# Optimization experiments

Measured on AMD Instinct MI355X. Metric: run time of the kernel, lower is better.

Reference implementation:

```python
import jax, jax.numpy as jnp
import numpy as np

N_ITEMS = 100000
EMB = 128
LAYERS = 3
N_EDGES = 1600000


def setup_inputs() -> dict:
    key = jax.random.key(0)
    k1, k2, k3, k4, k5 = jax.random.split(key, 5)
    embedding = jax.random.normal(k1, (N_ITEMS, EMB), dtype=jnp.float32)
    adj_vals = jax.random.uniform(k2, (N_EDGES,), dtype=jnp.float32)
    # per-layer Linear(emb, emb, bias=False) weights, torch default init scale ~ 1/sqrt(fan_in)
    weights = jax.random.normal(k3, (LAYERS, EMB, EMB), dtype=jnp.float32) / np.sqrt(EMB)
    rows = jax.random.randint(k4, (N_EDGES,), 0, N_ITEMS, dtype=jnp.int32)
    cols = jax.random.randint(k5, (N_EDGES,), 0, N_ITEMS, dtype=jnp.int32)
    return {"embedding": embedding, "adj_vals": adj_vals, "weights": weights,
            "rows": rows, "cols": cols}


def reference(embedding, adj_vals, weights, rows, cols):
    n = embedding.shape[0]
    layers = weights.shape[0]
    h = embedding
    acc = embedding  # final[0] = layer-0 embedding
    for i in range(layers):
        # Linear(bias=False): x @ W^T
        h = h @ weights[i].T
        # sparse.mm: out[r] = sum_e vals[e] * h[cols[e]] for edges with rows[e]==r
        msg = adj_vals[:, None] * h[cols]            # [E, D]
        h = jax.ops.segment_sum(msg, rows, num_segments=n)  # [N, D]
        # F.normalize(p=2, dim=-1): appended to final, but the UN-normalized h feeds the next layer
        norm = jnp.maximum(jnp.sqrt(jnp.sum(h * h, axis=-1, keepdims=True)), 1e-12)
        acc = acc + h / norm
    return acc / (layers + 1)
```

## Files before the change

kernel.cpp:

```cpp
#include <hip/hip_runtime.h>

#define N_ITEMS 100000
#define EMB     128
#define N_EDGES 1600000
#define NLAYERS 3
#define RCAP    48

typedef unsigned short u16;
typedef unsigned int   u32;
typedef __attribute__((ext_vector_type(8))) short short8;
typedef __attribute__((ext_vector_type(4))) float f32x4;

__device__ __forceinline__ float bf2f(u16 u) {
    union { u32 i; float f; } v; v.i = (u32)u << 16; return v.f;
}
__device__ __forceinline__ u16 f2bf(float f) {
    union { float f; u32 i; } v; v.f = f;
    u32 b = v.i;
    return (u16)((b + 0x7FFFu + ((b >> 16) & 1u)) >> 16);
}


__global__ __launch_bounds__(256) void fill_k(const int* __restrict__ rows,
                                              const int* __restrict__ cols,
                                              const float* __restrict__ vals,
                                              int* __restrict__ cnt,
                                              int2* __restrict__ bucket) {
    int e = blockIdx.x * 256 + threadIdx.x;
    if (e < N_EDGES) {
        int r = rows[e];
        int p = atomicAdd(&cnt[r], 1);
        if (p < RCAP) {
            bucket[(size_t)r * RCAP + p] = make_int2(cols[e], __float_as_int(vals[e]));
        }
    }
}


__global__ __launch_bounds__(256) void wconv_k(const float* __restrict__ W,
                                               u16* __restrict__ Wb) {
    int i = blockIdx.x * 256 + threadIdx.x;
    if (i < NLAYERS * EMB * EMB) Wb[i] = f2bf(W[i]);
}


__global__ __launch_bounds__(256) void init_k(const float4* __restrict__ emb,
                                              float4* __restrict__ out,
                                              ushort4* __restrict__ ebf) {
    int i = blockIdx.x * 256 + threadIdx.x;
    float4 v = emb[i];
    out[i] = make_float4(v.x * 0.25f, v.y * 0.25f, v.z * 0.25f, v.w * 0.25f);
    ushort4 u;
    u.x = f2bf(v.x); u.y = f2bf(v.y); u.z = f2bf(v.z); u.w = f2bf(v.w);
    ebf[i] = u;
}


__global__ __launch_bounds__(256) void gemm_k(const u16* __restrict__ in,
                                              const u16* __restrict__ Wb,
                                              u16* __restrict__ out) {
    __shared__ u16 Wl[128 * 136];
    int t = threadIdx.x;
    {
        int j = t >> 1, c0 = (t & 1) * 64;
        const short8* src = (const short8*)(Wb + j * 128 + c0);
        #pragma unroll
        for (int q = 0; q < 8; q++) {
            *(short8*)&Wl[j * 136 + c0 + q * 8] = src[q];
        }
    }
    __syncthreads();

    int l = t & 63, w = t >> 6;
    int g = l >> 4, r16 = l & 15;

    int rowA = blockIdx.x * 64 + w * 16 + r16;
    if (rowA > N_ITEMS - 1) rowA = N_ITEMS - 1;

    short8 a[4];
    #pragma unroll
    for (int kk = 0; kk < 4; kk++) {
        a[kk] = *(const short8*)(in + (size_t)rowA * 128 + kk * 32 + g * 8);
    }

    int rowD0 = blockIdx.x * 64 + w * 16 + g * 4;
    #pragma unroll
    for (int jt = 0; jt < 8; jt++) {
        f32x4 acc = {0.f, 0.f, 0.f, 0.f};
        int rb = jt * 16 + r16;
        #pragma unroll
        for (int kk = 0; kk < 4; kk++) {
            short8 b = *(const short8*)&Wl[rb * 136 + kk * 32 + g * 8];
            acc = __builtin_amdgcn_mfma_f32_16x16x32_bf16(a[kk], b, acc, 0, 0, 0);
        }
        int col = jt * 16 + r16;
        #pragma unroll
        for (int i = 0; i < 4; i++) {
            int row = rowD0 + i;
            if (row < N_ITEMS) out[(size_t)row * 128 + col] = f2bf(acc[i]);
        }
    }
}


template <bool WHN>
__global__ __launch_bounds__(256) void spmm_k(const u16* __restrict__ h,
                                              const int* __restrict__ cnt,
                                              const int2* __restrict__ bucket,
                                              u16* __restrict__ hn,
                                              float* __restrict__ acc) {
    int wid = (blockIdx.x * 256 + threadIdx.x) >> 6;
    int lane = threadIdx.x & 63;
    if (wid >= N_ITEMS) return;
    int n = cnt[wid];
    if (n > RCAP) n = RCAP;
    int2 my = make_int2(0, 0);
    if (lane < n) my = bucket[(size_t)wid * RCAP + lane];

    const ushort2* hb = (const ushort2*)h;
    float a0 = 0.f, a1 = 0.f;
    int j = 0;
    for (; j + 4 <= n; j += 4) {
        int   c0 = __shfl(my.x, j),     c1 = __shfl(my.x, j + 1);
        int   c2 = __shfl(my.x, j + 2), c3 = __shfl(my.x, j + 3);
        float v0 = __int_as_float(__shfl(my.y, j));
        float v1 = __int_as_float(__shfl(my.y, j + 1));
        float v2 = __int_as_float(__shfl(my.y, j + 2));
        float v3 = __int_as_float(__shfl(my.y, j + 3));
        ushort2 u0 = hb[(size_t)c0 * 64 + lane];
        ushort2 u1 = hb[(size_t)c1 * 64 + lane];
        ushort2 u2 = hb[(size_t)c2 * 64 + lane];
        ushort2 u3 = hb[(size_t)c3 * 64 + lane];
        a0 += v0 * bf2f(u0.x); a1 += v0 * bf2f(u0.y);
        a0 += v1 * bf2f(u1.x); a1 += v1 * bf2f(u1.y);
        a0 += v2 * bf2f(u2.x); a1 += v2 * bf2f(u2.y);
        a0 += v3 * bf2f(u3.x); a1 += v3 * bf2f(u3.y);
    }
    for (; j < n; j++) {
        int   c0 = __shfl(my.x, j);
        float v0 = __int_as_float(__shfl(my.y, j));
        ushort2 u0 = hb[(size_t)c0 * 64 + lane];
        a0 += v0 * bf2f(u0.x); a1 += v0 * bf2f(u0.y);
    }

    float ss = a0 * a0 + a1 * a1;
    #pragma unroll
    for (int off = 32; off > 0; off >>= 1) ss += __shfl_xor(ss, off);
    float inv = 0.25f / fmaxf(sqrtf(ss), 1e-12f);
    if (WHN) {
        ushort2 o;
        o.x = f2bf(a0);
        o.y = f2bf(a1);
        ((ushort2*)hn)[(size_t)wid * 64 + lane] = o;
    }
    float2* ap = (float2*)acc;
    size_t ai = (size_t)wid * 64 + lane;
    float2 o = ap[ai];
    o.x += a0 * inv;
    o.y += a1 * inv;
    ap[ai] = o;
}


extern "C" void kernel_launch(void* const* d_in, const int* in_sizes, int n_in,
                              void* d_out, int out_size, void* d_ws, size_t ws_size,
                              hipStream_t stream) {
    const float* emb  = (const float*)d_in[0];
    const float* vals = (const float*)d_in[1];
    const float* W    = (const float*)d_in[2];
    const int*   rows = (const int*)d_in[3];
    const int*   cols = (const int*)d_in[4];
    float* out = (float*)d_out;

    char* ws = (char*)d_ws;
    size_t off = 0;
    auto alloc = [&](size_t bytes) -> void* {
        void* p = ws + off;
        off = (off + bytes + 255) & ~(size_t)255;
        return p;
    };
    u16*  ebf    = (u16*)alloc((size_t)N_ITEMS * 128 * 2);
    u16*  hA     = (u16*)alloc((size_t)N_ITEMS * 128 * 2);
    u16*  hB     = (u16*)alloc((size_t)N_ITEMS * 128 * 2);
    int2* bucket = (int2*)alloc((size_t)N_ITEMS * RCAP * 8);
    int*  cnt    = (int*)alloc((size_t)N_ITEMS * 4);
    u16*  Wbf    = (u16*)alloc((size_t)NLAYERS * EMB * EMB * 2);

    hipMemsetAsync(cnt, 0, (size_t)N_ITEMS * 4, stream);
    fill_k<<<(N_EDGES + 255) / 256, 256, 0, stream>>>(rows, cols, vals, cnt, bucket);

    wconv_k<<<(NLAYERS * EMB * EMB + 255) / 256, 256, 0, stream>>>(W, Wbf);

    init_k<<<(N_ITEMS * 128 / 4) / 256, 256, 0, stream>>>((const float4*)emb,
                                                          (float4*)out, (ushort4*)ebf);

    const u16* cur = ebf;
    for (int L = 0; L < NLAYERS; L++) {
        gemm_k<<<(N_ITEMS + 63) / 64, 256, 0, stream>>>(cur, Wbf + (size_t)L * EMB * EMB, hB);
        if (L < NLAYERS - 1)
            spmm_k<true><<<N_ITEMS / 4, 256, 0, stream>>>(hB, cnt, bucket, hA, out);
        else
            spmm_k<false><<<N_ITEMS / 4, 256, 0, stream>>>(hB, cnt, bucket, hA, out);
        cur = hA;
    }
}
```

Measured before the change: 489.0 us.

## Build compact CSR via two-level binned sort and defer accumulation to merge kernel

Replaces the per-row global-atomic bucket fill with a coarse shared-memory binning pass by 256-row groups, then a per-bin local counting sort that produces a compact CSR with row starts and counts. The first GEMM reads fp32 embeddings directly, which removes the init kernel. The spmm no longer read-modify-writes the fp32 output each layer; it stores the bf16 hidden state and a per-row inverse norm, and one final merge kernel combines everything. The goals are fewer global atomics, less scattered writes during preprocessing, and less fp32 output traffic. The cost is two extra kernels, more workspace, and a silent truncation if any bin overflows CAP_BIN.

```diff
diff --git a/kernel.cpp b/kernel.cpp
--- a/kernel.cpp
+++ b/kernel.cpp
@@ -4,7 +4,8 @@
 #define EMB     128
 #define N_EDGES 1600000
 #define NLAYERS 3
-#define RCAP    48
+#define NBINS   391
+#define CAP_BIN 4608
 
 typedef unsigned short u16;
 typedef unsigned int   u32;
@@ -21,18 +22,79 @@
 }
 
 
-__global__ __launch_bounds__(256) void fill_k(const int* __restrict__ rows,
-                                              const int* __restrict__ cols,
-                                              const float* __restrict__ vals,
-                                              int* __restrict__ cnt,
-                                              int2* __restrict__ bucket) {
-    int e = blockIdx.x * 256 + threadIdx.x;
-    if (e < N_EDGES) {
+__global__ __launch_bounds__(256) void fill_coarse_k(const int* __restrict__ rows,
+                                                     const int* __restrict__ cols,
+                                                     const float* __restrict__ vals,
+                                                     int* __restrict__ bin_cnt,
+                                                     int2* __restrict__ binbuf) {
+    __shared__ int lcnt[NBINS];
+    __shared__ int lbase[NBINS];
+    int t = threadIdx.x;
+    for (int d = t; d < NBINS; d += 256) lcnt[d] = 0;
+    __syncthreads();
+    int chunk = (N_EDGES + gridDim.x - 1) / gridDim.x;
+    int e0 = blockIdx.x * chunk;
+    int e1 = e0 + chunk; if (e1 > N_EDGES) e1 = N_EDGES;
+    for (int e = e0 + t; e < e1; e += 256) {
+        atomicAdd(&lcnt[rows[e] >> 8], 1);
+    }
+    __syncthreads();
+    for (int d = t; d < NBINS; d += 256) {
+        int c = lcnt[d];
+        lbase[d] = c ? atomicAdd(&bin_cnt[d], c) : 0;
+        lcnt[d] = 0;
+    }
+    __syncthreads();
+    for (int e = e0 + t; e < e1; e += 256) {
         int r = rows[e];
-        int p = atomicAdd(&cnt[r], 1);
-        if (p < RCAP) {
-            bucket[(size_t)r * RCAP + p] = make_int2(cols[e], __float_as_int(vals[e]));
-        }
+        int d = r >> 8;
+        int p = lbase[d] + atomicAdd(&lcnt[d], 1);
+        if (p < CAP_BIN) {
+            int meta = ((r & 255) << 17) | cols[e];
+            binbuf[(size_t)d * CAP_BIN + p] = make_int2(meta, __float_as_int(vals[e]));
+        }
+    }
+}
+
+
+__global__ __launch_bounds__(256) void fill_fine_k(const int* __restrict__ bin_cnt,
+                                                   const int2* __restrict__ binbuf,
+                                                   int* __restrict__ cnt_g,
+                                                   int* __restrict__ rstart_g,
+                                                   int2* __restrict__ csr) {
+    __shared__ int lcnt[256], loff[256], lcur[256], ltmp[256];
+    int b = blockIdx.x, t = threadIdx.x;
+    int ne = bin_cnt[b]; if (ne > CAP_BIN) ne = CAP_BIN;
+    const int2* src = binbuf + (size_t)b * CAP_BIN;
+    lcnt[t] = 0;
+    __syncthreads();
+    for (int i = t; i < ne; i += 256) {
+        atomicAdd(&lcnt[src[i].x >> 17], 1);
+    }
+    __syncthreads();
+    int v = lcnt[t];
+    ltmp[t] = v;
+    __syncthreads();
+    for (int off = 1; off < 256; off <<= 1) {
+        int x = (t >= off) ? ltmp[t - off] : 0;
+        __syncthreads();
+        ltmp[t] += x;
+        __syncthreads();
+    }
+    loff[t] = ltmp[t] - v;
+    lcur[t] = 0;
+    int row = b * 256 + t;
+    if (row < N_ITEMS) {
+        cnt_g[row] = v;
+        rstart_g[row] = b * CAP_BIN + loff[t];
+    }
+    __syncthreads();
+    for (int i = t; i < ne; i += 256) {
+        int2 ev = src[i];
+        int rlow = ev.x >> 17;
+        int col = ev.x & 0x1FFFF;
+        int pos = loff[rlow] + atomicAdd(&lcur[rlow], 1);
+        csr[(size_t)b * CAP_BIN + pos] = make_int2(col, ev.y);
     }
 }
 
@@ -44,19 +106,8 @@
 }
 
 
-__global__ __launch_bounds__(256) void init_k(const float4* __restrict__ emb,
-                                              float4* __restrict__ out,
-                                              ushort4* __restrict__ ebf) {
-    int i = blockIdx.x * 256 + threadIdx.x;
-    float4 v = emb[i];
-    out[i] = make_float4(v.x * 0.25f, v.y * 0.25f, v.z * 0.25f, v.w * 0.25f);
-    ushort4 u;
-    u.x = f2bf(v.x); u.y = f2bf(v.y); u.z = f2bf(v.z); u.w = f2bf(v.w);
-    ebf[i] = u;
-}
-
-
-__global__ __launch_bounds__(256) void gemm_k(const u16* __restrict__ in,
+template <bool F32IN>
+__global__ __launch_bounds__(256) void gemm_k(const void* __restrict__ inp,
                                               const u16* __restrict__ Wb,
                                               u16* __restrict__ out) {
     __shared__ u16 Wl[128 * 136];
@@ -78,9 +129,25 @@
     if (rowA > N_ITEMS - 1) rowA = N_ITEMS - 1;
 
     short8 a[4];
-    #pragma unroll
-    for (int kk = 0; kk < 4; kk++) {
-        a[kk] = *(const short8*)(in + (size_t)rowA * 128 + kk * 32 + g * 8);
+    if (F32IN) {
+        const float* inf = (const float*)inp + (size_t)rowA * 128;
+        #pragma unroll
+        for (int kk = 0; kk < 4; kk++) {
+            float4 p0 = *(const float4*)(inf + kk * 32 + g * 8);
+            float4 p1 = *(const float4*)(inf + kk * 32 + g * 8 + 4);
+            short8 s;
+            s[0] = (short)f2bf(p0.x); s[1] = (short)f2bf(p0.y);
+            s[2] = (short)f2bf(p0.z); s[3] = (short)f2bf(p0.w);
+            s[4] = (short)f2bf(p1.x); s[5] = (short)f2bf(p1.y);
+            s[6] = (short)f2bf(p1.z); s[7] = (short)f2bf(p1.w);
+            a[kk] = s;
+        }
+    } else {
+        const u16* inb = (const u16*)inp + (size_t)rowA * 128;
+        #pragma unroll
+        for (int kk = 0; kk < 4; kk++) {
+            a[kk] = *(const short8*)(inb + kk * 32 + g * 8);
+        }
     }
 
     int rowD0 = blockIdx.x * 64 + w * 16 + g * 4;
@@ -90,8 +157,8 @@
         int rb = jt * 16 + r16;
         #pragma unroll
         for (int kk = 0; kk < 4; kk++) {
-            short8 b = *(const short8*)&Wl[rb * 136 + kk * 32 + g * 8];
-            acc = __builtin_amdgcn_mfma_f32_16x16x32_bf16(a[kk], b, acc, 0, 0, 0);
+            short8 bfr = *(const short8*)&Wl[rb * 136 + kk * 32 + g * 8];
+            acc = __builtin_amdgcn_mfma_f32_16x16x32_bf16(a[kk], bfr, acc, 0, 0, 0);
         }
         int col = jt * 16 + r16;
         #pragma unroll
@@ -103,19 +170,19 @@
 }
 
 
-template <bool WHN>
 __global__ __launch_bounds__(256) void spmm_k(const u16* __restrict__ h,
+                                              const int* __restrict__ rstart,
                                               const int* __restrict__ cnt,
-                                              const int2* __restrict__ bucket,
+                                              const int2* __restrict__ csr,
                                               u16* __restrict__ hn,
-                                              float* __restrict__ acc) {
+                                              float* __restrict__ inv) {
     int wid = (blockIdx.x * 256 + threadIdx.x) >> 6;
     int lane = threadIdx.x & 63;
     if (wid >= N_ITEMS) return;
+    int s = rstart[wid];
     int n = cnt[wid];
-    if (n > RCAP) n = RCAP;
     int2 my = make_int2(0, 0);
-    if (lane < n) my = bucket[(size_t)wid * RCAP + lane];
+    if (lane < n) my = csr[(size_t)s + lane];
 
     const ushort2* hb = (const ushort2*)h;
     float a0 = 0.f, a1 = 0.f;
@@ -146,19 +213,33 @@
     float ss = a0 * a0 + a1 * a1;
     #pragma unroll
     for (int off = 32; off > 0; off >>= 1) ss += __shfl_xor(ss, off);
-    float inv = 0.25f / fmaxf(sqrtf(ss), 1e-12f);
-    if (WHN) {
-        ushort2 o;
-        o.x = f2bf(a0);
-        o.y = f2bf(a1);
-        ((ushort2*)hn)[(size_t)wid * 64 + lane] = o;
-    }
-    float2* ap = (float2*)acc;
-    size_t ai = (size_t)wid * 64 + lane;
-    float2 o = ap[ai];
-    o.x += a0 * inv;
-    o.y += a1 * inv;
-    ap[ai] = o;
+    ushort2 o;
+    o.x = f2bf(a0);
+    o.y = f2bf(a1);
+    ((ushort2*)hn)[(size_t)wid * 64 + lane] = o;
+    if (lane == 0) inv[wid] = 1.0f / fmaxf(sqrtf(ss), 1e-12f);
+}
+
+
+__global__ __launch_bounds__(256) void merge_k(const float4* __restrict__ emb4,
+                                               const ushort4* __restrict__ h1,
+                                               const ushort4* __restrict__ h2,
+                                               const ushort4* __restrict__ h3,
+                                               const float* __restrict__ inv1,
+                                               const float* __restrict__ inv2,
+                                               const float* __restrict__ inv3,
+                                               float4* __restrict__ out4) {
+    int i = blockIdx.x * 256 + threadIdx.x;
+    int row = i >> 5;
+    float i1 = inv1[row], i2 = inv2[row], i3 = inv3[row];
+    float4 e = emb4[i];
+    ushort4 a = h1[i], b = h2[i], c = h3[i];
+    float4 o;
+    o.x = 0.25f * (e.x + bf2f(a.x) * i1 + bf2f(b.x) * i2 + bf2f(c.x) * i3);
+    o.y = 0.25f * (e.y + bf2f(a.y) * i1 + bf2f(b.y) * i2 + bf2f(c.y) * i3);
+    o.z = 0.25f * (e.z + bf2f(a.z) * i1 + bf2f(b.z) * i2 + bf2f(c.z) * i3);
+    o.w = 0.25f * (e.w + bf2f(a.w) * i1 + bf2f(b.w) * i2 + bf2f(c.w) * i3);
+    out4[i] = o;
 }
 
 
@@ -179,28 +260,43 @@
         off = (off + bytes + 255) & ~(size_t)255;
         return p;
     };
-    u16*  ebf    = (u16*)alloc((size_t)N_ITEMS * 128 * 2);
-    u16*  hA     = (u16*)alloc((size_t)N_ITEMS * 128 * 2);
-    u16*  hB     = (u16*)alloc((size_t)N_ITEMS * 128 * 2);
-    int2* bucket = (int2*)alloc((size_t)N_ITEMS * RCAP * 8);
-    int*  cnt    = (int*)alloc((size_t)N_ITEMS * 4);
-    u16*  Wbf    = (u16*)alloc((size_t)NLAYERS * EMB * EMB * 2);
-
-    hipMemsetAsync(cnt, 0, (size_t)N_ITEMS * 4, stream);
-    fill_k<<<(N_EDGES + 255) / 256, 256, 0, stream>>>(rows, cols, vals, cnt, bucket);
+    size_t arena_sz = (size_t)N_ITEMS * 128 * 2;
+    size_t bin_sz   = (size_t)NBINS * CAP_BIN * 8;
+    char* arena = (char*)alloc(arena_sz > bin_sz ? arena_sz : bin_sz);
+    int2* binbuf = (int2*)arena;
+    u16*  gbuf   = (u16*)arena;
+
+    u16*  hn0     = (u16*)alloc((size_t)N_ITEMS * 128 * 2);
+    u16*  hn1     = (u16*)alloc((size_t)N_ITEMS * 128 * 2);
+    u16*  hn2     = (u16*)alloc((size_t)N_ITEMS * 128 * 2);
+    int2* csr     = (int2*)alloc((size_t)NBINS * CAP_BIN * 8);
+    int*  bin_cnt = (int*)alloc((size_t)NBINS * 4);
+    int*  cnt_g   = (int*)alloc((size_t)N_ITEMS * 4);
+    int*  rstart  = (int*)alloc((size_t)N_ITEMS * 4);
+    float* inv0   = (float*)alloc((size_t)N_ITEMS * 4);
+    float* inv1   = (float*)alloc((size_t)N_ITEMS * 4);
+    float* inv2   = (float*)alloc((size_t)N_ITEMS * 4);
+    u16*  Wbf     = (u16*)alloc((size_t)NLAYERS * EMB * EMB * 2);
+
+    hipMemsetAsync(bin_cnt, 0, (size_t)NBINS * 4, stream);
+    fill_coarse_k<<<512, 256, 0, stream>>>(rows, cols, vals, bin_cnt, binbuf);
+    fill_fine_k<<<NBINS, 256, 0, stream>>>(bin_cnt, binbuf, cnt_g, rstart, csr);
 
     wconv_k<<<(NLAYERS * EMB * EMB + 255) / 256, 256, 0, stream>>>(W, Wbf);
 
-    init_k<<<(N_ITEMS * 128 / 4) / 256, 256, 0, stream>>>((const float4*)emb,
-                                                          (float4*)out, (ushort4*)ebf);
-
-    const u16* cur = ebf;
+    u16* hn[3] = {hn0, hn1, hn2};
+    float* inv[3] = {inv0, inv1, inv2};
+    const void* cur = emb;
     for (int L = 0; L < NLAYERS; L++) {
-        gemm_k<<<(N_ITEMS + 63) / 64, 256, 0, stream>>>(cur, Wbf + (size_t)L * EMB * EMB, hB);
-        if (L < NLAYERS - 1)
-            spmm_k<true><<<N_ITEMS / 4, 256, 0, stream>>>(hB, cnt, bucket, hA, out);
+        if (L == 0)
+            gemm_k<true><<<(N_ITEMS + 63) / 64, 256, 0, stream>>>(cur, Wbf, gbuf);
         else
-            spmm_k<false><<<N_ITEMS / 4, 256, 0, stream>>>(hB, cnt, bucket, hA, out);
-        cur = hA;
-    }
-}
+            gemm_k<false><<<(N_ITEMS + 63) / 64, 256, 0, stream>>>(cur, Wbf + (size_t)L * EMB * EMB, gbuf);
+        spmm_k<<<N_ITEMS / 4, 256, 0, stream>>>(gbuf, rstart, cnt_g, csr, hn[L], inv[L]);
+        cur = hn[L];
+    }
+
+    merge_k<<<(N_ITEMS * 128 / 4) / 256, 256, 0, stream>>>(
+        (const float4*)emb, (const ushort4*)hn0, (const ushort4*)hn1,
+        (const ushort4*)hn2, inv0, inv1, inv2, (float4*)out);
+}
```

Result: faster. 441.1 us (-9.8%).
